# Performance work log

Measured on AMD Instinct MI355X. Metric: run time of the kernel, lower is better.

Reference implementation:

```python
import jax, jax.numpy as jnp
import numpy as np

SEQ, BATCH, IN_DIM, HID = 512, 128, 1024, 1024

def setup_inputs() -> dict:
    key = jax.random.key(0)
    k1, k2, k3, k4 = jax.random.split(key, 4)
    scale = 0.02  # keep gate pre-activations in a sane range
    return {
        "inputs": jax.random.normal(k1, (SEQ, BATCH, IN_DIM), dtype=jnp.float32),
        "proj_W": jax.random.normal(k2, (4 * HID, IN_DIM + HID), dtype=jnp.float32) * scale,
        "proj_b": jax.random.normal(k3, (4 * HID,), dtype=jnp.float32) * scale,
        "qgate_W": jax.random.normal(k4, (HID, HID), dtype=jnp.float32) * scale,
    }

def reference(inputs, proj_W, proj_b, qgate_W):
    # inputs: [S, B, I]; proj_W: [4H, I+H]; qgate_W: [H, H]
    S, B, I = inputs.shape
    H = qgate_W.shape[0]
    Wx = proj_W[:, :I]   # [4H, I]
    Wh = proj_W[:, I:]   # [4H, H]
    # Precompute the input part of proj(cat([x, hx])) for all timesteps (same math).
    x_proj = jnp.einsum('sbi,gi->sbg', inputs, Wx) + proj_b  # [S, B, 4H]

    qWt = qgate_W.T
    def qgate(z):
        return jax.nn.sigmoid(z @ qWt)

    def step(carry, xp):
        hx, cx = carry
        gates = xp + hx @ Wh.T  # [B, 4H]
        f_in, i_in, g_in, o_in = jnp.split(gates, 4, axis=-1)
        # mixed/quantum mode: shared quantum gate, then outer nonlinearity (sigmoid of sigmoid, tanh of sigmoid)
        f = jax.nn.sigmoid(qgate(f_in))
        i = jax.nn.sigmoid(qgate(i_in))
        g = jnp.tanh(qgate(g_in))
        o = jax.nn.sigmoid(qgate(o_in))
        cx = f * cx + i * g
        hx = o * jnp.tanh(cx)
        return (hx, cx), hx

    init = (jnp.zeros((B, H), inputs.dtype), jnp.zeros((B, H), inputs.dtype))
    (hx, cx), outs = jax.lax.scan(step, init, x_proj)
    return outs, hx, cx
```

## Files before the change

kernel.cpp:

```cpp
#include <hip/hip_runtime.h>

typedef unsigned short ushort_t;
typedef __attribute__((ext_vector_type(4))) float f32x4;
typedef __attribute__((ext_vector_type(8))) __bf16 bf16x8;

#define SEQ   512
#define BATCH 128
#define HID   1024
#define G4    4096
#define CHUNK 64
#define BH    (BATCH*HID)
#define NBLK  256
#define FLAG_STRIDE 32
#define SCAN_LDS (131072 + 32768)

__device__ __forceinline__ ushort_t f2bf(float f) {
  unsigned u = __float_as_uint(f);
  u += 0x7FFFu + ((u >> 16) & 1u);
  return (ushort_t)(u >> 16);
}
__device__ __forceinline__ float bf2f(ushort_t h) {
  return __uint_as_float(((unsigned)h) << 16);
}
__device__ __forceinline__ float sigm(float x) { return 1.0f / (1.0f + __expf(-x)); }
__device__ __forceinline__ float ftanh(float x) {
  float xc = fminf(fmaxf(x, -15.f), 15.f);
  float t = __expf(2.f * xc);
  return (t - 1.f) / (t + 1.f);
}

__device__ __forceinline__ void lds16(const ushort_t* g, ushort_t* l) {
  __builtin_amdgcn_global_load_lds(
      (const __attribute__((address_space(1))) unsigned int*)g,
      (__attribute__((address_space(3))) unsigned int*)l, 16, 0, 0);
}
__device__ __forceinline__ void lds16c(const ushort_t* g, ushort_t* l) {
  __builtin_amdgcn_global_load_lds(
      (const __attribute__((address_space(1))) unsigned int*)g,
      (__attribute__((address_space(3))) unsigned int*)l, 16, 0, 0x11);
}

__global__ void cast_f32_bf16(const float* __restrict__ in, ushort_t* __restrict__ out, int n4) {
  int i = blockIdx.x * blockDim.x + threadIdx.x;
  if (i < n4) {
    float4 v = ((const float4*)in)[i];
    union { ushort_t u[4]; uint2 v2; } o;
    o.u[0] = f2bf(v.x); o.u[1] = f2bf(v.y); o.u[2] = f2bf(v.z); o.u[3] = f2bf(v.w);
    ((uint2*)out)[i] = o.v2;
  }
}

__global__ __launch_bounds__(256) void transpose_cast(const float* __restrict__ pw, ushort_t* __restrict__ pwt) {
  __shared__ float tile[32][33];
  int bx = blockIdx.x, by = blockIdx.y;
  int tx = threadIdx.x & 31, ty = threadIdx.x >> 5;
  for (int i = 0; i < 32; i += 8)
    tile[ty + i][tx] = pw[(size_t)(by*32 + ty + i)*2048 + bx*32 + tx];
  __syncthreads();
  for (int i = 0; i < 32; i += 8) {
    int r = ty + i;
    pwt[(size_t)(bx*32 + r)*4096 + by*32 + tx] = f2bf(tile[tx][r]);
  }
}

__global__ void bias_fold(const float* __restrict__ qW, const float* __restrict__ pb, float* __restrict__ b2) {
  int r = blockIdx.x;
  int j = r & (HID-1), gb = r & ~(HID-1);
  float s = 0.f;
  for (int k = threadIdx.x; k < HID; k += 64)
    s += qW[(size_t)j*HID + k] * pb[gb + k];
  for (int off = 32; off; off >>= 1) s += __shfl_down(s, off, 64);
  if (threadIdx.x == 0) b2[r] = s;
}

__global__ __launch_bounds__(256) void gemm128(
    const ushort_t* __restrict__ A, int lda, unsigned arow_mask,
    const ushort_t* __restrict__ B, int ldb, unsigned bko_mask,
    const float* __restrict__ bias, ushort_t* __restrict__ C, int ldc, int K)
{
  __shared__ __align__(16) ushort_t Al[128*64];
  __shared__ __align__(16) ushort_t Bl[128*64];
  const int tid = threadIdx.x, wv = tid >> 6, ln = tid & 63;
  const int bn = blockIdx.x, bm = blockIdx.y;
  const int bko = (int)(((unsigned)(bm << 7)) & bko_mask);
  const int m0 = (wv & 1) << 6, n0 = (wv >> 1) << 6;
  f32x4 acc[4][4] = {};
  for (int k0 = 0; k0 < K; k0 += 64) {
    for (int rr = 0; rr < 4; ++rr) {
      int r0 = (rr << 5) + (wv << 3);
      unsigned ga = ((unsigned)((bm << 7) + r0 + (ln >> 3))) & arow_mask;
      lds16(A + (size_t)ga*lda + k0 + ((ln & 7) << 3), &Al[r0 << 6]);
      unsigned gbr = (unsigned)((bn << 7) + r0 + (ln >> 3));
      lds16(B + (size_t)gbr*ldb + bko + k0 + ((ln & 7) << 3), &Bl[r0 << 6]);
    }
    __syncthreads();
    for (int kk = 0; kk < 64; kk += 32) {
      const int lrow = ln & 15, lk = kk + ((ln >> 4) << 3);
      bf16x8 af[4], bfr[4];
      for (int i = 0; i < 4; ++i) af[i]  = *(const bf16x8*)&Al[((m0 + (i << 4) + lrow) << 6) + lk];
      for (int j = 0; j < 4; ++j) bfr[j] = *(const bf16x8*)&Bl[((n0 + (j << 4) + lrow) << 6) + lk];
      for (int i = 0; i < 4; ++i)
        for (int j = 0; j < 4; ++j)
          acc[i][j] = __builtin_amdgcn_mfma_f32_16x16x32_bf16(af[i], bfr[j], acc[i][j], 0, 0, 0);
    }
    __syncthreads();
  }
  for (int i = 0; i < 4; ++i)
    for (int j = 0; j < 4; ++j) {
      int col = (bn << 7) + n0 + (j << 4) + (ln & 15);
      float bv = bias ? bias[col] : 0.f;
      for (int r = 0; r < 4; ++r) {
        int row = (bm << 7) + m0 + (i << 4) + ((ln >> 4) << 2) + r;
        C[(size_t)row*ldc + col] = f2bf(acc[i][j][r] + bv);
      }
    }
}

__global__ __launch_bounds__(256, 1) void qlstm_scan(
    const ushort_t* __restrict__ P,
    const ushort_t* __restrict__ W2,
    ushort_t* __restrict__ hxb,
    float* __restrict__ cxg,
    float* __restrict__ outc,
    int t0,
    unsigned* __restrict__ flags)
{
  extern __shared__ __align__(16) ushort_t lds[];
  ushort_t* Ul = lds;
  ushort_t* Ar = lds + 65536;
  float*    sm = (float*)(lds + 65536);

  const int tid = threadIdx.x, wv = tid >> 6, ln = tid & 63;
  const int rblk = blockIdx.x & 3, cblk = blockIdx.x >> 2;
  unsigned* gflags = flags + (size_t)rblk*64*FLAG_STRIDE;

  for (int ck = 0; ck < 8; ++ck)
    for (int rr = 0; rr < 4; ++rr) {
      int lr = rr*16 + wv*4 + (ln >> 4);
      int grow = ((lr >> 4) << 10) + cblk*16 + (lr & 15);
      int gcol = ck*128 + (((ln & 15) ^ (lr & 7)) << 3);
      lds16(W2 + (size_t)grow*2048 + 1024 + gcol, &Ul[ck*8192 + (rr*16 + wv*4)*128]);
    }

  const int b_loc = tid >> 3;
  const int j0    = (tid & 7) << 1;
  const size_t ci = (size_t)(rblk*32 + b_loc)*1024 + cblk*16 + j0;
  float2 cxr = *(const float2*)&cxg[ci];

  auto stageA = [&](int slot, int k0, const ushort_t* hxR) {
    #pragma unroll
    for (int rr = 0; rr < 2; ++rr) {
      int row = rr*16 + wv*4 + (ln >> 4);
      int gcol = ((ln & 15) ^ (row & 7)) << 3;
      lds16c(hxR + (size_t)(rblk*32 + row)*1024 + k0 + gcol,
             &Ar[slot*4096 + (rr*16 + wv*4)*128]);
    }
  };
  auto load_pv = [&](int tl, float* pv) {
    #pragma unroll
    for (int i = 0; i < 2; ++i)
      #pragma unroll
      for (int r = 0; r < 4; ++r) {
        int bl = i*16 + ((ln >> 4) << 2) + r;
        pv[i*4+r] = bf2f(P[(size_t)(tl*128 + rblk*32 + bl)*4096 + (wv << 10) + cblk*16 + (ln & 15)]);
      }
  };

  float pv[8];
  load_pv(0, pv);

  for (int tl = 0; tl < CHUNK; ++tl) {
    const int t = t0 + tl;
    const ushort_t* hxR = hxb + (size_t)(t % 3)*BH;
    ushort_t*       hxW = hxb + (size_t)((t + 1) % 3)*BH;

    f32x4 acc0 = {}, acc1 = {};
    stageA(0, 0, hxR);
    stageA(1, 128, hxR);
    stageA(2, 256, hxR);

    #define COMPUTE_CK(CK)                                                         \
      {                                                                            \
        const int aslot = (CK) & 3;                                                \
        _Pragma("unroll")                                                          \
        for (int k4 = 0; k4 < 4; ++k4) {                                           \
          int s = k4*4 + (ln >> 4);                                                \
          int ar0 = ln & 15, ar1 = 16 + (ln & 15);                                 \
          int brow = wv*16 + (ln & 15);                                            \
          bf16x8 a0 = *(const bf16x8*)&Ar[aslot*4096 + ar0*128 + ((s ^ (ar0 & 7)) << 3)]; \
          bf16x8 a1 = *(const bf16x8*)&Ar[aslot*4096 + ar1*128 + ((s ^ (ar1 & 7)) << 3)]; \
          bf16x8 bb = *(const bf16x8*)&Ul[(CK)*8192 + brow*128 + ((s ^ (brow & 7)) << 3)]; \
          acc0 = __builtin_amdgcn_mfma_f32_16x16x32_bf16(a0, bb, acc0, 0, 0, 0);   \
          acc1 = __builtin_amdgcn_mfma_f32_16x16x32_bf16(a1, bb, acc1, 0, 0, 0);   \
        }                                                                          \
      }
    #define STEP_CK(CK, WN, DOSTAGE)                                               \
      asm volatile("s_waitcnt vmcnt(" #WN ")" ::: "memory");                       \
      __builtin_amdgcn_s_barrier();                                                \
      if (DOSTAGE) stageA(((CK)+3) & 3, ((CK)+3)*128, hxR);                        \
      COMPUTE_CK(CK)

    STEP_CK(0, 4, 1) STEP_CK(1, 4, 1) STEP_CK(2, 4, 1)
    STEP_CK(3, 4, 1) STEP_CK(4, 4, 1)
    STEP_CK(5, 4, 0) STEP_CK(6, 2, 0) STEP_CK(7, 0, 0)
    #undef STEP_CK
    #undef COMPUTE_CK

    #pragma unroll
    for (int i = 0; i < 2; ++i)
      #pragma unroll
      for (int r = 0; r < 4; ++r) {
        int bl = i*16 + ((ln >> 4) << 2) + r;
        float v = (i ? acc1[r] : acc0[r]) + pv[i*4+r];
        sm[wv*512 + bl*16 + (ln & 15)] = sigm(v);
      }
    __syncthreads();
    float2 h2;
    {
      const float2* sm2 = (const float2*)sm;
      int e = b_loc*8 + (j0 >> 1);
      float2 sF = sm2[0*256 + e], sI = sm2[1*256 + e];
      float2 sG = sm2[2*256 + e], sO = sm2[3*256 + e];
      float f0 = sigm(sF.x), i0 = sigm(sI.x), g0 = ftanh(sG.x), o0 = sigm(sO.x);
      float f1 = sigm(sF.y), i1 = sigm(sI.y), g1 = ftanh(sG.y), o1 = sigm(sO.y);
      float cn0 = f0*cxr.x + i0*g0, cn1 = f1*cxr.y + i1*g1;
      float h0 = o0*ftanh(cn0),     h1 = o1*ftanh(cn1);
      cxr.x = cn0; cxr.y = cn1;
      h2.x = h0; h2.y = h1;
      unsigned hp = (unsigned)f2bf(h0) | ((unsigned)f2bf(h1) << 16);
      __hip_atomic_store((unsigned*)&hxW[ci], hp,
                         __ATOMIC_RELAXED, __HIP_MEMORY_SCOPE_AGENT);
    }

    if (tl != CHUNK - 1) {
      const unsigned gen = (unsigned)(t + 1);
      asm volatile("s_waitcnt vmcnt(0)" ::: "memory");
      __syncthreads();
      if (tid == 0)
        __hip_atomic_store(gflags + (size_t)cblk*FLAG_STRIDE, gen,
                           __ATOMIC_RELAXED, __HIP_MEMORY_SCOPE_AGENT);
      *(float2*)&outc[(size_t)tl*BH + ci] = h2;
      float pvn[8];
      load_pv(tl + 1, pvn);
      if (tid < 64) {
        int it = 0;
        for (;;) {
          unsigned a = __hip_atomic_load(gflags + (size_t)tid*FLAG_STRIDE,
                                         __ATOMIC_RELAXED, __HIP_MEMORY_SCOPE_AGENT);
          if (__all(a >= gen)) break;
          if ((++it & 255) == 0) __builtin_amdgcn_fence(__ATOMIC_ACQUIRE, "agent");
          __builtin_amdgcn_s_sleep(1);
        }
      }
      __syncthreads();
      #pragma unroll
      for (int q = 0; q < 8; ++q) pv[q] = pvn[q];
    } else {
      *(float2*)&outc[(size_t)tl*BH + ci] = h2;
    }
  }
  *(float2*)&cxg[ci] = cxr;
}

extern "C" void kernel_launch(void* const* d_in, const int* in_sizes, int n_in,
                              void* d_out, int out_size, void* d_ws, size_t ws_size,
                              hipStream_t stream) {
  const float* x  = (const float*)d_in[0];
  const float* pW = (const float*)d_in[1];
  const float* pb = (const float*)d_in[2];
  const float* qW = (const float*)d_in[3];
  float* out = (float*)d_out;

  char* w = (char*)d_ws;
  auto carve = [&](size_t bytes) { char* p = w; w += (bytes + 255) & ~(size_t)255; return p; };
  ushort_t* qWbf = (ushort_t*)carve((size_t)HID*HID*2);
  ushort_t* pWt  = (ushort_t*)carve((size_t)2048*4096*2);
  ushort_t* W2   = (ushort_t*)carve((size_t)4096*2048*2);
  float*    b2   = (float*)   carve((size_t)4096*4);
  ushort_t* hxb  = (ushort_t*)carve((size_t)3*BH*2);
  float*    cxws = (float*)   carve((size_t)BH*4);
  unsigned* flags= (unsigned*)carve((size_t)NBLK*FLAG_STRIDE*4);
  ushort_t* xbf  = (ushort_t*)carve((size_t)CHUNK*BATCH*HID*2);
  ushort_t* Pc   = (ushort_t*)carve((size_t)CHUNK*BATCH*G4*2);

  (void)hipFuncSetAttribute((const void*)qlstm_scan,
                            hipFuncAttributeMaxDynamicSharedMemorySize, SCAN_LDS);

  cast_f32_bf16<<<(HID*HID/4 + 255)/256, 256, 0, stream>>>(qW, qWbf, HID*HID/4);
  transpose_cast<<<dim3(64, 128), 256, 0, stream>>>(pW, pWt);
  bias_fold<<<4096, 64, 0, stream>>>(qW, pb, b2);
  gemm128<<<dim3(16, 32), 256, 0, stream>>>(qWbf, 1024, 1023u, pWt, 4096, ~1023u, nullptr, W2, 2048, 1024);

  hipMemsetAsync(hxb, 0, (size_t)BH*2, stream);
  hipMemsetAsync(cxws, 0, (size_t)BH*4, stream);
  hipMemsetAsync(flags, 0, (size_t)NBLK*FLAG_STRIDE*4, stream);

  for (int c = 0; c < SEQ/CHUNK; ++c) {
    cast_f32_bf16<<<(CHUNK*BATCH*HID/4 + 255)/256, 256, 0, stream>>>(
        x + (size_t)c*CHUNK*BATCH*HID, xbf, CHUNK*BATCH*HID/4);
    gemm128<<<dim3(G4/128, CHUNK*BATCH/128), 256, 0, stream>>>(
        xbf, 1024, ~0u, W2, 2048, 0u, b2, Pc, 4096, 1024);

    const ushort_t* Pa = Pc; const ushort_t* W2a = W2;
    ushort_t* hxa = hxb; float* cxa = cxws;
    float* outa = out + (size_t)c*CHUNK*BH;
    int t0 = c*CHUNK; unsigned* fla = flags;
    void* args[7] = { &Pa, &W2a, &hxa, &cxa, &outa, &t0, &fla };
    hipLaunchCooperativeKernel((const void*)qlstm_scan, dim3(NBLK), dim3(256),
                               args, SCAN_LDS, stream);
  }
  hipMemcpyAsync(out + (size_t)SEQ*BH,      out + (size_t)(SEQ-1)*BH, (size_t)BH*4,
                 hipMemcpyDeviceToDevice, stream);
  hipMemcpyAsync(out + (size_t)SEQ*BH + BH, cxws, (size_t)BH*4,
                 hipMemcpyDeviceToDevice, stream);
}
```

Baseline: 3.322 ms.

## Replace per-chunk input GEMM with 256x256 tiled, double-buffered MFMA kernel

After: 2.995 ms. 9.8% less time.

```diff
diff --git a/kernel.cpp b/kernel.cpp
--- a/kernel.cpp
+++ b/kernel.cpp
@@ -13,6 +13,7 @@
 #define NBLK  256
 #define FLAG_STRIDE 32
 #define SCAN_LDS (131072 + 32768)
+#define GEMM256_LDS 131072
 
 __device__ __forceinline__ ushort_t f2bf(float f) {
   unsigned u = __float_as_uint(f);
@@ -116,6 +117,105 @@
     }
 }
 
+__global__ __launch_bounds__(512) void gemm256(
+    const ushort_t* __restrict__ A, const ushort_t* __restrict__ B,
+    const float* __restrict__ bias, ushort_t* __restrict__ C)
+{
+  extern __shared__ __align__(16) ushort_t lds[];
+  ushort_t* LA = lds;
+  ushort_t* LB = lds + 32768;
+  const int tid = threadIdx.x, wv8 = tid >> 6, ln = tid & 63;
+  const int wm = wv8 >> 2, wn = wv8 & 3;
+  const int bn = blockIdx.x, bm = blockIdx.y;
+  const int lr = ln & 15, lg = ln >> 4;
+
+  f32x4 acc[8][4] = {};
+  bf16x8 af[4][2], bfr[4][2];
+
+  auto stA = [&](int db, int half, int kt) {
+    ushort_t* d = LA + db*16384 + half*8192 + (wv8 << 9);
+    const int ce = ((ln & 7) ^ (ln >> 3)) << 3;
+    #pragma unroll
+    for (int p = 0; p < 2; ++p) {
+      int rr = half*128 + p*64 + (wv8 << 3) + (ln >> 3);
+      lds16(A + (size_t)(bm*256 + rr)*1024 + kt*64 + ce, d + p*4096);
+    }
+  };
+  auto stB = [&](int db, int half, int kt) {
+    ushort_t* d = LB + db*16384 + half*8192 + (wv8 << 9);
+    const int ce = ((ln & 7) ^ (ln >> 3)) << 3;
+    #pragma unroll
+    for (int p = 0; p < 2; ++p) {
+      int rr = half*128 + p*64 + (wv8 << 3) + (ln >> 3);
+      lds16(B + (size_t)(bn*256 + rr)*2048 + kt*64 + ce, d + p*4096);
+    }
+  };
+
+#define RD_A(DB, MQ) { _Pragma("unroll") for (int i_ = 0; i_ < 4; ++i_) { \
+    const int row_ = ((MQ)*4 + i_)*16 + lr; \
+    const ushort_t* b_ = &LA[(DB)*16384 + wm*8192 + row_*64]; \
+    af[i_][0] = *(const bf16x8*)&b_[ (lg << 3)       ^ ((lr & 7) << 3)]; \
+    af[i_][1] = *(const bf16x8*)&b_[((lg << 3) | 32) ^ ((lr & 7) << 3)]; } }
+
+#define RD_B(DB, NQ) { _Pragma("unroll") for (int j_ = 0; j_ < 2; ++j_) { \
+    const int row_ = (wn & 1)*64 + ((NQ)*2 + j_)*16 + lr; \
+    const ushort_t* b_ = &LB[(DB)*16384 + (wn >> 1)*8192 + row_*64]; \
+    bfr[(NQ)*2 + j_][0] = *(const bf16x8*)&b_[ (lg << 3)       ^ ((lr & 7) << 3)]; \
+    bfr[(NQ)*2 + j_][1] = *(const bf16x8*)&b_[((lg << 3) | 32) ^ ((lr & 7) << 3)]; } }
+
+#define QUAD(MQ, NQ) \
+  __builtin_amdgcn_s_setprio(1); \
+  { _Pragma("unroll") for (int i_ = 0; i_ < 4; ++i_) \
+      _Pragma("unroll") for (int j_ = 0; j_ < 2; ++j_) \
+        _Pragma("unroll") for (int k_ = 0; k_ < 2; ++k_) \
+          acc[(MQ)*4 + i_][(NQ)*2 + j_] = __builtin_amdgcn_mfma_f32_16x16x32_bf16( \
+              af[i_][k_], bfr[(NQ)*2 + j_][k_], acc[(MQ)*4 + i_][(NQ)*2 + j_], 0, 0, 0); } \
+  __builtin_amdgcn_s_setprio(0);
+
+#define BAR() __builtin_amdgcn_s_barrier()
+#define LGK0() do { asm volatile("s_waitcnt lgkmcnt(0)" ::: "memory"); \
+                    __builtin_amdgcn_sched_barrier(0); } while (0)
+#define VM4() do { asm volatile("s_waitcnt vmcnt(4)" ::: "memory"); \
+                   __builtin_amdgcn_sched_barrier(0); } while (0)
+
+  stA(0,0,0); stA(0,1,0); stB(0,0,0); stB(0,1,0); stB(1,0,1); stB(1,1,1);
+  asm volatile("s_waitcnt vmcnt(4)" ::: "memory");
+  BAR();
+
+  for (int i = 0; i < 8; ++i) {
+    const int k1 = 2*i + 1, k2 = 2*i + 2, k3 = 2*i + 3;
+    RD_A(0,0); RD_B(0,0); stA(1,0,k1);            BAR(); LGK0(); QUAD(0,0); BAR();
+    RD_B(0,1); stA(1,1,k1);                       BAR(); LGK0(); QUAD(0,1); BAR();
+    RD_A(0,1); if (k2 < 16) stB(0,0,k2);          BAR(); LGK0(); QUAD(1,0); BAR();
+    if (k2 < 16) stB(0,1,k2);                     BAR();         QUAD(1,1); VM4(); BAR();
+    RD_A(1,0); RD_B(1,0); if (k2 < 16) stA(0,0,k2); BAR(); LGK0(); QUAD(0,0); BAR();
+    RD_B(1,1); if (k2 < 16) stA(0,1,k2);          BAR(); LGK0(); QUAD(0,1); BAR();
+    RD_A(1,1); if (k3 < 16) stB(1,0,k3);          BAR(); LGK0(); QUAD(1,0); BAR();
+    if (k3 < 16) stB(1,1,k3);                     BAR();         QUAD(1,1); VM4(); BAR();
+  }
+
+  const int crow0 = bm*256 + wm*128;
+  const int ccol0 = bn*256 + wn*64;
+  #pragma unroll
+  for (int m = 0; m < 8; ++m)
+    #pragma unroll
+    for (int n = 0; n < 4; ++n) {
+      int col = ccol0 + n*16 + lr;
+      float bv = bias[col];
+      #pragma unroll
+      for (int r = 0; r < 4; ++r) {
+        int row = crow0 + m*16 + lg*4 + r;
+        C[(size_t)row*4096 + col] = f2bf(acc[m][n][r] + bv);
+      }
+    }
+#undef RD_A
+#undef RD_B
+#undef QUAD
+#undef BAR
+#undef LGK0
+#undef VM4
+}
+
 __global__ __launch_bounds__(256, 1) void qlstm_scan(
     const ushort_t* __restrict__ P,
     const ushort_t* __restrict__ W2,
@@ -285,6 +385,8 @@
 
   (void)hipFuncSetAttribute((const void*)qlstm_scan,
                             hipFuncAttributeMaxDynamicSharedMemorySize, SCAN_LDS);
+  (void)hipFuncSetAttribute((const void*)gemm256,
+                            hipFuncAttributeMaxDynamicSharedMemorySize, GEMM256_LDS);
 
   cast_f32_bf16<<<(HID*HID/4 + 255)/256, 256, 0, stream>>>(qW, qWbf, HID*HID/4);
   transpose_cast<<<dim3(64, 128), 256, 0, stream>>>(pW, pWt);
@@ -298,8 +400,8 @@
   for (int c = 0; c < SEQ/CHUNK; ++c) {
     cast_f32_bf16<<<(CHUNK*BATCH*HID/4 + 255)/256, 256, 0, stream>>>(
         x + (size_t)c*CHUNK*BATCH*HID, xbf, CHUNK*BATCH*HID/4);
-    gemm128<<<dim3(G4/128, CHUNK*BATCH/128), 256, 0, stream>>>(
-        xbf, 1024, ~0u, W2, 2048, 0u, b2, Pc, 4096, 1024);
+    gemm256<<<dim3(G4/256, CHUNK*BATCH/256), 512, GEMM256_LDS, stream>>>(
+        xbf, W2, b2, Pc);
 
     const ushort_t* Pa = Pc; const ushort_t* W2a = W2;
     ushort_t* hxa = hxb; float* cxa = cxws;
```

## Fuse input projection into persistent scan kernel, overlapping next chunk with recurrence

Applied to the files above, without the earlier changes.

Measured after the change: 11.80 ms. +255.4%, slower.

```diff
diff --git a/kernel.cpp b/kernel.cpp
--- a/kernel.cpp
+++ b/kernel.cpp
@@ -27,6 +27,19 @@
   float xc = fminf(fmaxf(x, -15.f), 15.f);
   float t = __expf(2.f * xc);
   return (t - 1.f) / (t + 1.f);
+}
+__device__ __forceinline__ unsigned pkbf(float a, float b) {
+  unsigned r;
+  asm("v_cvt_pk_bf16_f32 %0, %1, %2" : "=v"(r) : "v"(a), "v"(b));
+  return r;
+}
+__device__ __forceinline__ float lo16(unsigned u){ return __uint_as_float(u << 16); }
+__device__ __forceinline__ float hi16(unsigned u){ return __uint_as_float(u & 0xffff0000u); }
+__device__ __forceinline__ bf16x8 cvt8(float4 lo, float4 hi) {
+  union { unsigned u[4]; bf16x8 v; } r;
+  r.u[0] = pkbf(lo.x, lo.y); r.u[1] = pkbf(lo.z, lo.w);
+  r.u[2] = pkbf(hi.x, hi.y); r.u[3] = pkbf(hi.z, hi.w);
+  return r.v;
 }
 
 __device__ __forceinline__ void lds16(const ushort_t* g, ushort_t* l) {
@@ -117,12 +130,12 @@
 }
 
 __global__ __launch_bounds__(256, 1) void qlstm_scan(
-    const ushort_t* __restrict__ P,
+    unsigned* __restrict__ Pp,
     const ushort_t* __restrict__ W2,
+    const float* __restrict__ x,
+    const float* __restrict__ b2,
     ushort_t* __restrict__ hxb,
-    float* __restrict__ cxg,
-    float* __restrict__ outc,
-    int t0,
+    float* __restrict__ out,
     unsigned* __restrict__ flags)
 {
   extern __shared__ __align__(16) ushort_t lds[];
@@ -132,20 +145,56 @@
 
   const int tid = threadIdx.x, wv = tid >> 6, ln = tid & 63;
   const int rblk = blockIdx.x & 3, cblk = blockIdx.x >> 2;
+  const int lr = ln & 15, lg = ln >> 4;
   unsigned* gflags = flags + (size_t)rblk*64*FLAG_STRIDE;
 
   for (int ck = 0; ck < 8; ++ck)
     for (int rr = 0; rr < 4; ++rr) {
-      int lr = rr*16 + wv*4 + (ln >> 4);
-      int grow = ((lr >> 4) << 10) + cblk*16 + (lr & 15);
-      int gcol = ck*128 + (((ln & 15) ^ (lr & 7)) << 3);
+      int lrr = rr*16 + wv*4 + (ln >> 4);
+      int grow = ((lrr >> 4) << 10) + cblk*16 + (lrr & 15);
+      int gcol = ck*128 + (((ln & 15) ^ (lrr & 7)) << 3);
       lds16(W2 + (size_t)grow*2048 + 1024 + gcol, &Ul[ck*8192 + (rr*16 + wv*4)*128]);
     }
 
   const int b_loc = tid >> 3;
   const int j0    = (tid & 7) << 1;
   const size_t ci = (size_t)(rblk*32 + b_loc)*1024 + cblk*16 + j0;
-  float2 cxr = *(const float2*)&cxg[ci];
+  float2 cxr; cxr.x = 0.f; cxr.y = 0.f;
+
+  const float bv = b2[(wv << 10) + cblk*16 + lr];
+  const ushort_t* vrow = W2 + (size_t)((wv << 10) + cblk*16 + lr)*2048;
+  unsigned* pslot = Pp + ((((size_t)blockIdx.x*CHUNK)*4 + wv)*64 + lg*16 + lr)*4;
+
+  auto slab = [&](int cn, int tl) {
+    const float* xa = x + ((size_t)(cn*CHUNK + tl)*BATCH + rblk*32 + lr)*HID;
+    const float* xb = xa + 16*HID;
+    f32x4 p0 = {}, p1 = {};
+    #pragma unroll 2
+    for (int ks = 0; ks < 32; ++ks) {
+      int k = ks*32 + lg*8;
+      float4 a0l = *(const float4*)(xa + k);
+      float4 a0h = *(const float4*)(xa + k + 4);
+      float4 a1l = *(const float4*)(xb + k);
+      float4 a1h = *(const float4*)(xb + k + 4);
+      union { uint4 u; bf16x8 v; } bb; bb.u = *(const uint4*)(vrow + k);
+      bf16x8 a0 = cvt8(a0l, a0h), a1 = cvt8(a1l, a1h);
+      p0 = __builtin_amdgcn_mfma_f32_16x16x32_bf16(a0, bb.v, p0, 0, 0, 0);
+      p1 = __builtin_amdgcn_mfma_f32_16x16x32_bf16(a1, bb.v, p1, 0, 0, 0);
+    }
+    uint4 pk;
+    pk.x = pkbf(p0[0] + bv, p0[1] + bv);
+    pk.y = pkbf(p0[2] + bv, p0[3] + bv);
+    pk.z = pkbf(p1[0] + bv, p1[1] + bv);
+    pk.w = pkbf(p1[2] + bv, p1[3] + bv);
+    *(uint4*)(pslot + (size_t)tl*1024) = pk;
+  };
+  auto load_pv = [&](int tl, float* pv) {
+    uint4 u = *(const uint4*)(pslot + (size_t)tl*1024);
+    pv[0] = lo16(u.x); pv[1] = hi16(u.x);
+    pv[2] = lo16(u.y); pv[3] = hi16(u.y);
+    pv[4] = lo16(u.z); pv[5] = hi16(u.z);
+    pv[6] = lo16(u.w); pv[7] = hi16(u.w);
+  };
 
   auto stageA = [&](int slot, int k0, const ushort_t* hxR) {
     #pragma unroll
@@ -156,21 +205,15 @@
              &Ar[slot*4096 + (rr*16 + wv*4)*128]);
     }
   };
-  auto load_pv = [&](int tl, float* pv) {
-    #pragma unroll
-    for (int i = 0; i < 2; ++i)
-      #pragma unroll
-      for (int r = 0; r < 4; ++r) {
-        int bl = i*16 + ((ln >> 4) << 2) + r;
-        pv[i*4+r] = bf2f(P[(size_t)(tl*128 + rblk*32 + bl)*4096 + (wv << 10) + cblk*16 + (ln & 15)]);
-      }
-  };
+
+  for (int tl = 0; tl < CHUNK; ++tl) slab(0, tl);
+  asm volatile("s_waitcnt vmcnt(0)" ::: "memory");
 
   float pv[8];
   load_pv(0, pv);
 
-  for (int tl = 0; tl < CHUNK; ++tl) {
-    const int t = t0 + tl;
+  for (int t = 0; t < SEQ; ++t) {
+    const int tl = t & (CHUNK - 1);
     const ushort_t* hxR = hxb + (size_t)(t % 3)*BH;
     ushort_t*       hxW = hxb + (size_t)((t + 1) % 3)*BH;
 
@@ -232,16 +275,17 @@
                          __ATOMIC_RELAXED, __HIP_MEMORY_SCOPE_AGENT);
     }
 
-    if (tl != CHUNK - 1) {
+    if (t != SEQ - 1) {
       const unsigned gen = (unsigned)(t + 1);
       asm volatile("s_waitcnt vmcnt(0)" ::: "memory");
       __syncthreads();
       if (tid == 0)
         __hip_atomic_store(gflags + (size_t)cblk*FLAG_STRIDE, gen,
                            __ATOMIC_RELAXED, __HIP_MEMORY_SCOPE_AGENT);
-      *(float2*)&outc[(size_t)tl*BH + ci] = h2;
+      *(float2*)&out[(size_t)t*BH + ci] = h2;
       float pvn[8];
-      load_pv(tl + 1, pvn);
+      load_pv((t + 1) & (CHUNK - 1), pvn);
+      if (t < SEQ - CHUNK) slab((t >> 6) + 1, tl);
       if (tid < 64) {
         int it = 0;
         for (;;) {
@@ -253,13 +297,15 @@
         }
       }
       __syncthreads();
+      asm volatile("s_waitcnt vmcnt(0)" ::: "memory");
       #pragma unroll
       for (int q = 0; q < 8; ++q) pv[q] = pvn[q];
     } else {
-      *(float2*)&outc[(size_t)tl*BH + ci] = h2;
+      *(float2*)&out[(size_t)t*BH + ci] = h2;
+      *(float2*)&out[(size_t)SEQ*BH + ci] = h2;
     }
   }
-  *(float2*)&cxg[ci] = cxr;
+  *(float2*)&out[(size_t)(SEQ + 1)*BH + ci] = cxr;
 }
 
 extern "C" void kernel_launch(void* const* d_in, const int* in_sizes, int n_in,
@@ -278,10 +324,8 @@
   ushort_t* W2   = (ushort_t*)carve((size_t)4096*2048*2);
   float*    b2   = (float*)   carve((size_t)4096*4);
   ushort_t* hxb  = (ushort_t*)carve((size_t)3*BH*2);
-  float*    cxws = (float*)   carve((size_t)BH*4);
   unsigned* flags= (unsigned*)carve((size_t)NBLK*FLAG_STRIDE*4);
-  ushort_t* xbf  = (ushort_t*)carve((size_t)CHUNK*BATCH*HID*2);
-  ushort_t* Pc   = (ushort_t*)carve((size_t)CHUNK*BATCH*G4*2);
+  unsigned* Pp   = (unsigned*)carve((size_t)NBLK*CHUNK*1024*4);
 
   (void)hipFuncSetAttribute((const void*)qlstm_scan,
                             hipFuncAttributeMaxDynamicSharedMemorySize, SCAN_LDS);
@@ -292,25 +336,11 @@
   gemm128<<<dim3(16, 32), 256, 0, stream>>>(qWbf, 1024, 1023u, pWt, 4096, ~1023u, nullptr, W2, 2048, 1024);
 
   hipMemsetAsync(hxb, 0, (size_t)BH*2, stream);
-  hipMemsetAsync(cxws, 0, (size_t)BH*4, stream);
   hipMemsetAsync(flags, 0, (size_t)NBLK*FLAG_STRIDE*4, stream);
 
-  for (int c = 0; c < SEQ/CHUNK; ++c) {
-    cast_f32_bf16<<<(CHUNK*BATCH*HID/4 + 255)/256, 256, 0, stream>>>(
-        x + (size_t)c*CHUNK*BATCH*HID, xbf, CHUNK*BATCH*HID/4);
-    gemm128<<<dim3(G4/128, CHUNK*BATCH/128), 256, 0, stream>>>(
-        xbf, 1024, ~0u, W2, 2048, 0u, b2, Pc, 4096, 1024);
-
-    const ushort_t* Pa = Pc; const ushort_t* W2a = W2;
-    ushort_t* hxa = hxb; float* cxa = cxws;
-    float* outa = out + (size_t)c*CHUNK*BH;
-    int t0 = c*CHUNK; unsigned* fla = flags;
-    void* args[7] = { &Pa, &W2a, &hxa, &cxa, &outa, &t0, &fla };
-    hipLaunchCooperativeKernel((const void*)qlstm_scan, dim3(NBLK), dim3(256),
-                               args, SCAN_LDS, stream);
-  }
-  hipMemcpyAsync(out + (size_t)SEQ*BH,      out + (size_t)(SEQ-1)*BH, (size_t)BH*4,
-                 hipMemcpyDeviceToDevice, stream);
-  hipMemcpyAsync(out + (size_t)SEQ*BH + BH, cxws, (size_t)BH*4,
-                 hipMemcpyDeviceToDevice, stream);
-}
+  unsigned* Ppa = Pp; const ushort_t* W2a = W2; const float* xa = x;
+  const float* b2a = b2; ushort_t* hxa = hxb; float* outa = out; unsigned* fla = flags;
+  void* args[7] = { &Ppa, &W2a, &xa, &b2a, &hxa, &outa, &fla };
+  hipLaunchCooperativeKernel((const void*)qlstm_scan, dim3(NBLK), dim3(256),
+                             args, SCAN_LDS, stream);
+}
```
